# Kernel tuning notes

Hardware: AMD Instinct MI355X
Metric: run time of the kernel (lower is better)

## Reference

```python
import jax, jax.numpy as jnp
from jax import lax
import numpy as np

B, H, W, C = 4, 128, 128, 128   # C == d_route == n_heads, patch_len == H
OFFSET_RANGE = 5.0              # offset_range_factor == kernel == 5
SCALE = C ** -0.5               # self.scale_factor = d_route**-0.5
CYCLE = 168


def grid_sample_bilinear(img, grid):
    """torch.nn.functional.grid_sample(mode='bilinear', padding_mode='zeros', align_corners=False).
    img: (B,C,H,W); grid: (B,H,W,2) with (x,y) in [-1,1]."""
    Bn, Cn, Hn, Wn = img.shape
    xg = (grid[..., 0] + 1.0) * (Wn / 2.0) - 0.5
    yg = (grid[..., 1] + 1.0) * (Hn / 2.0) - 0.5
    x0 = jnp.floor(xg)
    y0 = jnp.floor(yg)
    img_flat = img.reshape(Bn, Cn, Hn * Wn)
    out = jnp.zeros_like(img)
    for xi in (x0, x0 + 1.0):
        for yi in (y0, y0 + 1.0):
            wgt = (1.0 - jnp.abs(xg - xi)) * (1.0 - jnp.abs(yg - yi))
            valid = (xi >= 0) & (xi <= Wn - 1) & (yi >= 0) & (yi <= Hn - 1)
            ix = jnp.clip(xi, 0, Wn - 1).astype(jnp.int32)
            iy = jnp.clip(yi, 0, Hn - 1).astype(jnp.int32)
            idx = (iy * Wn + ix).reshape(Bn, 1, -1)                      # (B,1,H*W)
            vals = jnp.take_along_axis(img_flat, idx, axis=2).reshape(Bn, Cn, Hn, Wn)
            out = out + vals * (wgt * valid.astype(img.dtype))[:, None, :, :]
    return out


def setup_inputs():
    key = jax.random.key(0)
    ks = jax.random.split(key, 12)
    s = C ** -0.5
    inp = {
        "x": jax.random.normal(ks[0], (B, H, W, C), dtype=jnp.float32),
        "cycle_index": jax.random.randint(ks[1], (B, 128), 0, CYCLE),  # dead path in cycle_mode='None'
        "Wq": jax.random.normal(ks[2], (C, C), dtype=jnp.float32) * s,
        "bq": jnp.zeros((C,), dtype=jnp.float32),
        "Wk": jax.random.normal(ks[3], (C, C), dtype=jnp.float32) * s,
        "bk": jnp.zeros((C,), dtype=jnp.float32),
        "Wv": jax.random.normal(ks[4], (C, C), dtype=jnp.float32) * s,
        "bv": jnp.zeros((C,), dtype=jnp.float32),
        "Wo": jax.random.normal(ks[5], (C, C), dtype=jnp.float32) * s,
        "bo": jnp.zeros((C,), dtype=jnp.float32),
        "Wc1": jax.random.normal(ks[6], (C, C, 5, 5), dtype=jnp.float32) * (1.0 / np.sqrt(C * 25)),
        "bc1": jnp.zeros((C,), dtype=jnp.float32),
        "Wc2": jax.random.normal(ks[7], (2, C), dtype=jnp.float32) * s,   # 1x1 conv, no bias
        "rel_bias": jax.random.normal(ks[8], (1, C, H, 1), dtype=jnp.float32) * 0.02,
    }
    return inp


def reference(x, cycle_index, Wq, bq, Wk, bk, Wv, bv, Wo, bo, Wc1, bc1, Wc2, rel_bias):
    Bn, Hn, Wn, Cn = x.shape
    xc = jnp.transpose(x, (0, 3, 1, 2))                                  # (B,C,H,W)
    # proj_q (1x1 conv) on x (cycle_mode='None')
    q = jnp.einsum('oc,bchw->bohw', Wq, xc) + bq[None, :, None, None]
    # proj_offset: 5x5 conv (pad 2) -> 1x1 conv to 2 channels, tanh * offset_range_factor
    c1 = lax.conv_general_dilated(q, Wc1, (1, 1), ((2, 2), (2, 2)),
                                  dimension_numbers=('NCHW', 'OIHW', 'NCHW')) + bc1[None, :, None, None]
    offset = jnp.tanh(jnp.einsum('oc,bchw->bohw', Wc2, c1)) * OFFSET_RANGE  # (B,2,H,W)
    # create_grid_like + normalize_grid (faithful, incl. x-coord normalized by H and vice versa)
    gx, gy = jnp.meshgrid(jnp.arange(Wn, dtype=x.dtype), jnp.arange(Hn, dtype=x.dtype), indexing='xy')
    grid = jnp.stack([gx, gy], axis=0)                                   # (2,H,W)
    vgrid = grid[None] + offset                                          # (B,2,H,W)
    gh = 2.0 * vgrid[:, 0] / max(Hn - 1, 1) - 1.0
    gw = 2.0 * vgrid[:, 1] / max(Wn - 1, 1) - 1.0
    sgrid = jnp.stack([gh, gw], axis=-1)                                 # (B,H,W,2) = (x,y) for grid_sample
    x_sampled = grid_sample_bilinear(xc, sgrid)                          # (B,C,H,W); n_groups=1 -> rearrange is identity
    k = (jnp.einsum('oc,bchw->bohw', Wk, x_sampled) + bk[None, :, None, None]).reshape(Bn * Cn, Hn, Wn)
    v = (jnp.einsum('oc,bchw->bohw', Wv, x_sampled) + bv[None, :, None, None] + rel_bias).reshape(Bn * Cn, Hn, Wn)
    qr = q.reshape(Bn * Cn, Hn, Wn)
    scores = jnp.einsum('bid,bjd->bij', qr, k) * SCALE                   # (B*C,H,H)
    attn = jax.nn.softmax(scores, axis=-1)
    out = jnp.einsum('bij,bjd->bid', attn, v)                            # (B*C,H,W)
    out = out.reshape(Bn, Hn, Wn, Cn)                                    # faithful raw reshape (as in original)
    return out @ Wo.T + bo
```

## Files before the change

kernel.cpp:

```cpp
#include <hip/hip_runtime.h>
#include <math.h>

#define IMG 16384

typedef short short4v __attribute__((ext_vector_type(4)));
typedef short short8  __attribute__((ext_vector_type(8)));
typedef float floatx4 __attribute__((ext_vector_type(4)));

__device__ __forceinline__ float4 ld4(const float* p) {
    return *reinterpret_cast<const float4*>(p);
}
__device__ __forceinline__ short f2bf(float f) {
    union { float f; unsigned u; } v; v.f = f;
    unsigned r = v.u + 0x7fffu + ((v.u >> 16) & 1u);
    return (short)(r >> 16);
}
__device__ __forceinline__ float bf2f(short s) {
    union { unsigned u; float f; } v;
    v.u = ((unsigned)(unsigned short)s) << 16;
    return v.f;
}

__launch_bounds__(256)
__global__ void k_wprep(const float* __restrict__ Wc1, const float* __restrict__ Wc2,
                        const float* __restrict__ bc1, const float* __restrict__ Wq,
                        const float* __restrict__ bq, const float* __restrict__ Wk,
                        const float* __restrict__ Wv, const float* __restrict__ Wo,
                        float* __restrict__ W2, float* __restrict__ cst,
                        float* __restrict__ b_eff, short* __restrict__ wbf) {
    const int t = threadIdx.x;
    if (blockIdx.x >= 50) {
        int i = (blockIdx.x - 50) * 256 + t;
        int base = i * 8;
        int sel = base >> 14, off = base & 16383;
        const float* s = (sel == 0) ? Wq : (sel == 1) ? Wk : (sel == 2) ? Wv : Wo;
        float4 a = ld4(s + off), b = ld4(s + off + 4);
        short8 o;
        o[0] = f2bf(a.x); o[1] = f2bf(a.y); o[2] = f2bf(a.z); o[3] = f2bf(a.w);
        o[4] = f2bf(b.x); o[5] = f2bf(b.y); o[6] = f2bf(b.z); o[7] = f2bf(b.w);
        *reinterpret_cast<short8*>(wbf + base) = o;
        return;
    }
    __shared__ float U[128];
    __shared__ float red[256];
    __shared__ float wc2[128];
    __shared__ float bql[128];
    const int tt = blockIdx.x;
    const int tch = tt / 25, tap = tt % 25;
    if (t < 128) { wc2[t] = Wc2[tch * 128 + t]; bql[t] = bq[t]; }
    __syncthreads();
    const int c = t & 127, half = t >> 7;
    float p = 0.f;
    for (int o = half * 64; o < half * 64 + 64; ++o)
        p += wc2[o] * Wc1[(o * 128 + c) * 25 + tap];
    red[half * 128 + c] = p;
    __syncthreads();
    if (t < 128) U[t] = red[t] + red[128 + t];
    __syncthreads();
    float p2 = 0.f;
    for (int cc = half * 64; cc < half * 64 + 64; ++cc)
        p2 += U[cc] * Wq[cc * 128 + c];
    red[half * 128 + c] = p2;
    __syncthreads();
    if (t < 128) W2[tt * 128 + t] = red[t] + red[128 + t];
    if (t < 128) red[t] = U[t] * bql[t];
    __syncthreads();
    if (t == 0) {
        float s = 0.f;
        for (int j = 0; j < 128; ++j) s += red[j];
        cst[tt] = s;
    }
    if (tap == 0) {
        __syncthreads();
        if (t < 128) red[t] = wc2[t] * bc1[t];
        __syncthreads();
        if (t == 0) {
            float s = 0.f;
            for (int j = 0; j < 128; ++j) s += red[j];
            b_eff[tch] = s;
        }
    }
}

__launch_bounds__(256)
__global__ void k_off(const float* __restrict__ x, const float* __restrict__ W2,
                      const float* __restrict__ cst, float* __restrict__ P,
                      short* __restrict__ x_bf) {
    __shared__ float Wlds[128 * 68];
    __shared__ float Alds[32 * 68];
    const int t = threadIdx.x;
    const int pg = t & 15, og = t >> 4;
    const int p0 = blockIdx.x * 64;
    const int b = p0 >> 14, pix0 = p0 & (IMG - 1);

    for (int id = t; id < 128 * 64; id += 256) {
        int k = id >> 6, o = id & 63;
        Wlds[k * 68 + o] = (o < 50) ? W2[o * 128 + k] : 0.f;
    }
    float acc[4][4];
#pragma unroll
    for (int i = 0; i < 4; ++i)
#pragma unroll
        for (int j = 0; j < 4; ++j) acc[i][j] = 0.f;

    for (int kc = 0; kc < 128; kc += 32) {
        __syncthreads();
#pragma unroll
        for (int rep = 0; rep < 2; ++rep) {
            int id = rep * 256 + t;
            int m = id >> 3, k4 = (id & 7) * 4;
            float4 v = ld4(x + (size_t)(p0 + m) * 128 + kc + k4);
            Alds[(k4 + 0) * 68 + m] = v.x;
            Alds[(k4 + 1) * 68 + m] = v.y;
            Alds[(k4 + 2) * 68 + m] = v.z;
            Alds[(k4 + 3) * 68 + m] = v.w;
            short4v s = {f2bf(v.x), f2bf(v.y), f2bf(v.z), f2bf(v.w)};
            *reinterpret_cast<short4v*>(x_bf + (size_t)(p0 + m) * 128 + kc + k4) = s;
        }
        __syncthreads();
#pragma unroll
        for (int k = 0; k < 32; ++k) {
            float4 a = *reinterpret_cast<float4*>(&Alds[k * 68 + 4 * pg]);
            float4 wv = *reinterpret_cast<float4*>(&Wlds[(kc + k) * 68 + 4 * og]);
            float av[4] = {a.x, a.y, a.z, a.w};
            float wf[4] = {wv.x, wv.y, wv.z, wv.w};
#pragma unroll
            for (int i = 0; i < 4; ++i)
#pragma unroll
                for (int j = 0; j < 4; ++j)
                    acc[i][j] = fmaf(av[i], wf[j], acc[i][j]);
        }
    }
    __syncthreads();
#pragma unroll
    for (int j = 0; j < 4; ++j) {
        int o = 4 * og + j;
        float c = (o < 50) ? cst[o] : 0.f;
        *reinterpret_cast<float4*>(&Wlds[o * 68 + 4 * pg]) =
            make_float4(acc[0][j] + c, acc[1][j] + c, acc[2][j] + c, acc[3][j] + c);
    }
    __syncthreads();
    for (int id = t; id < 50 * 16; id += 256) {
        int o = id >> 4, px4 = (id & 15) * 4;
        float4 v = *reinterpret_cast<float4*>(&Wlds[o * 68 + px4]);
        *reinterpret_cast<float4*>(P + ((size_t)(b * 50 + o)) * IMG + pix0 + px4) = v;
    }
}

__launch_bounds__(256, 2)
__global__ void k_fused2(const float* __restrict__ P, const float* __restrict__ b_eff,
                         const short* __restrict__ x_bf, const short* __restrict__ wbf,
                         const float* __restrict__ bq, const float* __restrict__ bk,
                         const float* __restrict__ bv, const float* __restrict__ rel,
                         short* __restrict__ q_bf, short* __restrict__ k_bf,
                         short* __restrict__ v_bf) {
    __shared__ __align__(16) char smem[62240];
    float* rowsP  = (float*)smem;
    short* xsT    = (short*)(smem + 26400);
    float* offs_l = (float*)(smem + 61216);

    const int t = threadIdx.x;
    const int w = t >> 6, l = t & 63, l15 = l & 15, quad = l >> 4;
    const int mh = w >> 1, nh = w & 1;
    const int bh = blockIdx.x;
    const int b = bh >> 7, h = bh & 127;

    for (int id = t; id < 1600; id += 256) {
        int o = id >> 5, q4 = (id & 31) * 4;
        int di = (o % 25) / 5;
        int r = h + di - 2;
        float4 v = make_float4(0.f, 0.f, 0.f, 0.f);
        if (r >= 0 && r < 128)
            v = ld4(P + ((size_t)(b * 50 + o)) * IMG + r * 128 + q4);
        *reinterpret_cast<float4*>(&rowsP[o * 132 + q4]) = v;
    }
    __syncthreads();
    {
        int wp = t & 127, tc = t >> 7;
        float acc = 0.f;
#pragma unroll
        for (int di = 0; di < 5; ++di)
#pragma unroll
            for (int dj = 0; dj < 5; ++dj) {
                int wj = wp + dj - 2;
                if (wj >= 0 && wj < 128)
                    acc += rowsP[(tc * 25 + di * 5 + dj) * 132 + wj];
            }
        offs_l[tc * 128 + wp] = tanhf(acc + b_eff[tc]) * 5.0f;
    }
    __syncthreads();

    for (int id = t; id < 2048; id += 256) {
        int px = id >> 4, c8 = id & 15;
        float ox = offs_l[px];
        float oy = offs_l[128 + px];
        float xg = ((float)px + ox) * (128.0f / 127.0f) - 0.5f;
        float yg = ((float)h  + oy) * (128.0f / 127.0f) - 0.5f;
        float x0f = floorf(xg), y0f = floorf(yg);
        float fx = xg - x0f, fy = yg - y0f;
        int x0 = (int)x0f, y0 = (int)y0f;
        float s[8];
#pragma unroll
        for (int r = 0; r < 8; ++r) s[r] = 0.f;
#pragma unroll
        for (int tap = 0; tap < 4; ++tap) {
            int xi = x0 + (tap & 1), yi = y0 + (tap >> 1);
            float wgt = ((tap & 1) ? fx : 1.f - fx) * ((tap >> 1) ? fy : 1.f - fy);
            if (xi >= 0 && xi < 128 && yi >= 0 && yi < 128) {
                short8 v = *reinterpret_cast<const short8*>(
                    x_bf + (((size_t)(b * 128 + yi)) * 128 + xi) * 128 + c8 * 8);
#pragma unroll
                for (int r = 0; r < 8; ++r) s[r] = fmaf(wgt, bf2f(v[r]), s[r]);
            }
        }
        short8 o;
#pragma unroll
        for (int r = 0; r < 8; ++r) o[r] = f2bf(s[r]);
        *reinterpret_cast<short8*>(&xsT[px * 136 + c8 * 8]) = o;
    }

    {
        const short* xr = x_bf + ((size_t)(b * 128 + h)) * 128 * 128;
        floatx4 acc[4][4];
#pragma unroll
        for (int im = 0; im < 4; ++im)
#pragma unroll
            for (int in = 0; in < 4; ++in)
                acc[im][in] = (floatx4){0.f, 0.f, 0.f, 0.f};
#pragma unroll
        for (int kc = 0; kc < 128; kc += 32) {
            short8 af[4], bf_[4];
#pragma unroll
            for (int im = 0; im < 4; ++im)
                af[im] = *reinterpret_cast<const short8*>(
                    xr + (mh * 64 + im * 16 + l15) * 128 + kc + quad * 8);
#pragma unroll
            for (int in = 0; in < 4; ++in)
                bf_[in] = *reinterpret_cast<const short8*>(
                    wbf + (nh * 64 + in * 16 + l15) * 128 + kc + quad * 8);
#pragma unroll
            for (int im = 0; im < 4; ++im)
#pragma unroll
                for (int in = 0; in < 4; ++in)
                    acc[im][in] = __builtin_amdgcn_mfma_f32_16x16x32_bf16(
                        af[im], bf_[in], acc[im][in], 0, 0, 0);
        }
#pragma unroll
        for (int in = 0; in < 4; ++in) {
            int o = nh * 64 + in * 16 + l15;
            float bb = bq[o];
#pragma unroll
            for (int im = 0; im < 4; ++im) {
                int px0 = mh * 64 + im * 16 + quad * 4;
                short4v s = {f2bf(acc[im][in][0] + bb), f2bf(acc[im][in][1] + bb),
                             f2bf(acc[im][in][2] + bb), f2bf(acc[im][in][3] + bb)};
                *reinterpret_cast<short4v*>(
                    q_bf + ((size_t)(b * 128 + o)) * IMG + h * 128 + px0) = s;
            }
        }
    }
    __syncthreads();

    {
        floatx4 ak[4][4], av[4][4];
#pragma unroll
        for (int im = 0; im < 4; ++im)
#pragma unroll
            for (int in = 0; in < 4; ++in) {
                ak[im][in] = (floatx4){0.f, 0.f, 0.f, 0.f};
                av[im][in] = (floatx4){0.f, 0.f, 0.f, 0.f};
            }
#pragma unroll
        for (int kc = 0; kc < 128; kc += 32) {
            short8 af[4], bk_[4], bv_[4];
#pragma unroll
            for (int im = 0; im < 4; ++im)
                af[im] = *reinterpret_cast<const short8*>(
                    &xsT[(mh * 64 + im * 16 + l15) * 136 + kc + quad * 8]);
#pragma unroll
            for (int in = 0; in < 4; ++in) {
                bk_[in] = *reinterpret_cast<const short8*>(
                    wbf + 16384 + (nh * 64 + in * 16 + l15) * 128 + kc + quad * 8);
                bv_[in] = *reinterpret_cast<const short8*>(
                    wbf + 32768 + (nh * 64 + in * 16 + l15) * 128 + kc + quad * 8);
            }
#pragma unroll
            for (int im = 0; im < 4; ++im)
#pragma unroll
                for (int in = 0; in < 4; ++in) {
                    ak[im][in] = __builtin_amdgcn_mfma_f32_16x16x32_bf16(
                        af[im], bk_[in], ak[im][in], 0, 0, 0);
                    av[im][in] = __builtin_amdgcn_mfma_f32_16x16x32_bf16(
                        af[im], bv_[in], av[im][in], 0, 0, 0);
                }
        }
#pragma unroll
        for (int in = 0; in < 4; ++in) {
            int o = nh * 64 + in * 16 + l15;
            float bbk = bk[o];
            float bbv = bv[o] + rel[o * 128 + h];
#pragma unroll
            for (int im = 0; im < 4; ++im) {
                int px0 = mh * 64 + im * 16 + quad * 4;
                size_t base = ((size_t)(b * 128 + o)) * IMG + h * 128 + px0;
                short4v sk = {f2bf(ak[im][in][0] + bbk), f2bf(ak[im][in][1] + bbk),
                              f2bf(ak[im][in][2] + bbk), f2bf(ak[im][in][3] + bbk)};
                short4v sv = {f2bf(av[im][in][0] + bbv), f2bf(av[im][in][1] + bbv),
                              f2bf(av[im][in][2] + bbv), f2bf(av[im][in][3] + bbv)};
                *reinterpret_cast<short4v*>(k_bf + base) = sk;
                *reinterpret_cast<short4v*>(v_bf + base) = sv;
            }
        }
    }
}

__launch_bounds__(256)
__global__ void k_attn3(const short* __restrict__ q_bf, const short* __restrict__ k_bf,
                        const short* __restrict__ v_bf, const short* __restrict__ WoB,
                        const float* __restrict__ bo, float* __restrict__ outp) {
    __shared__ __align__(16) short Pb[128 * 136];
    __shared__ __align__(16) short vT[128 * 136];
    __shared__ float redm[2 * 128];
    __shared__ float reds[2 * 128];

    const int t = threadIdx.x;
    const int w = t >> 6, l = t & 63, l15 = l & 15, quad = l >> 4;
    const int mh = w >> 1, nh = w & 1;
    const size_t hb = (size_t)blockIdx.x * IMG;
    const short* qp = q_bf + hb;
    const short* kp = k_bf + hb;
    const short* vp = v_bf + hb;

    for (int id = t; id < 2048; id += 256) {
        int j = id >> 4, seg = id & 15;
        short8 v8 = *reinterpret_cast<const short8*>(vp + j * 128 + seg * 8);
#pragma unroll
        for (int r = 0; r < 8; ++r)
            vT[(seg * 8 + r) * 136 + j] = v8[r];
    }

    floatx4 acc[4][4];
#pragma unroll
    for (int im = 0; im < 4; ++im)
#pragma unroll
        for (int in = 0; in < 4; ++in)
            acc[im][in] = (floatx4){0.f, 0.f, 0.f, 0.f};

#pragma unroll
    for (int kc = 0; kc < 128; kc += 32) {
        short8 af[4], bf_[4];
#pragma unroll
        for (int im = 0; im < 4; ++im)
            af[im] = *reinterpret_cast<const short8*>(
                qp + (mh * 64 + im * 16 + l15) * 128 + kc + quad * 8);
#pragma unroll
        for (int in = 0; in < 4; ++in)
            bf_[in] = *reinterpret_cast<const short8*>(
                kp + (nh * 64 + in * 16 + l15) * 128 + kc + quad * 8);
#pragma unroll
        for (int im = 0; im < 4; ++im)
#pragma unroll
            for (int in = 0; in < 4; ++in)
                acc[im][in] = __builtin_amdgcn_mfma_f32_16x16x32_bf16(
                    af[im], bf_[in], acc[im][in], 0, 0, 0);
    }

    const float scale = 0.08838834764831845f;
    float mloc[4][4];
#pragma unroll
    for (int im = 0; im < 4; ++im)
#pragma unroll
        for (int r = 0; r < 4; ++r) {
            float m = acc[im][0][r];
#pragma unroll
            for (int in = 1; in < 4; ++in) m = fmaxf(m, acc[im][in][r]);
            mloc[im][r] = m;
        }
#pragma unroll
    for (int mask = 1; mask < 16; mask <<= 1)
#pragma unroll
        for (int im = 0; im < 4; ++im)
#pragma unroll
            for (int r = 0; r < 4; ++r)
                mloc[im][r] = fmaxf(mloc[im][r], __shfl_xor(mloc[im][r], mask, 64));
    if (l15 == 0) {
#pragma unroll
        for (int im = 0; im < 4; ++im)
#pragma unroll
            for (int r = 0; r < 4; ++r)
                redm[nh * 128 + mh * 64 + im * 16 + quad * 4 + r] = mloc[im][r];
    }
    __syncthreads();
    float sloc[4][4];
#pragma unroll
    for (int im = 0; im < 4; ++im)
#pragma unroll
        for (int r = 0; r < 4; ++r) {
            int row = mh * 64 + im * 16 + quad * 4 + r;
            float m = fmaxf(redm[row], redm[128 + row]);
            float ss = 0.f;
#pragma unroll
            for (int in = 0; in < 4; ++in) {
                float e = __expf((acc[im][in][r] - m) * scale);
                acc[im][in][r] = e;
                ss += e;
            }
            sloc[im][r] = ss;
        }
#pragma unroll
    for (int mask = 1; mask < 16; mask <<= 1)
#pragma unroll
        for (int im = 0; im < 4; ++im)
#pragma unroll
            for (int r = 0; r < 4; ++r)
                sloc[im][r] += __shfl_xor(sloc[im][r], mask, 64);
    if (l15 == 0) {
#pragma unroll
        for (int im = 0; im < 4; ++im)
#pragma unroll
            for (int r = 0; r < 4; ++r)
                reds[nh * 128 + mh * 64 + im * 16 + quad * 4 + r] = sloc[im][r];
    }
    __syncthreads();
#pragma unroll
    for (int im = 0; im < 4; ++im)
#pragma unroll
        for (int r = 0; r < 4; ++r) {
            int row = mh * 64 + im * 16 + quad * 4 + r;
            float inv = 1.0f / (reds[row] + reds[128 + row]);
#pragma unroll
            for (int in = 0; in < 4; ++in) {
                int col = nh * 64 + in * 16 + l15;
                Pb[row * 136 + col] = f2bf(acc[im][in][r] * inv);
            }
        }
    __syncthreads();

#pragma unroll
    for (int im = 0; im < 4; ++im)
#pragma unroll
        for (int in = 0; in < 4; ++in)
            acc[im][in] = (floatx4){0.f, 0.f, 0.f, 0.f};
#pragma unroll
    for (int kc = 0; kc < 128; kc += 32) {
        short8 af[4], bf_[4];
#pragma unroll
        for (int im = 0; im < 4; ++im)
            af[im] = *reinterpret_cast<const short8*>(
                &Pb[(mh * 64 + im * 16 + l15) * 136 + kc + quad * 8]);
#pragma unroll
        for (int in = 0; in < 4; ++in)
            bf_[in] = *reinterpret_cast<const short8*>(
                &vT[(nh * 64 + in * 16 + l15) * 136 + kc + quad * 8]);
#pragma unroll
        for (int im = 0; im < 4; ++im)
#pragma unroll
            for (int in = 0; in < 4; ++in)
                acc[im][in] = __builtin_amdgcn_mfma_f32_16x16x32_bf16(
                    af[im], bf_[in], acc[im][in], 0, 0, 0);
    }
    __syncthreads();
#pragma unroll
    for (int im = 0; im < 4; ++im)
#pragma unroll
        for (int in = 0; in < 4; ++in) {
            int col = nh * 64 + in * 16 + l15;
#pragma unroll
            for (int r = 0; r < 4; ++r) {
                int row = mh * 64 + im * 16 + quad * 4 + r;
                Pb[row * 136 + col] = f2bf(acc[im][in][r]);
            }
        }
    __syncthreads();

    float bb[4];
#pragma unroll
    for (int in = 0; in < 4; ++in) bb[in] = bo[nh * 64 + in * 16 + l15];
#pragma unroll
    for (int im = 0; im < 4; ++im)
#pragma unroll
        for (int in = 0; in < 4; ++in)
            acc[im][in] = (floatx4){0.f, 0.f, 0.f, 0.f};
#pragma unroll
    for (int kc = 0; kc < 128; kc += 32) {
        short8 af[4], bf_[4];
#pragma unroll
        for (int im = 0; im < 4; ++im)
            af[im] = *reinterpret_cast<const short8*>(
                &Pb[(mh * 64 + im * 16 + l15) * 136 + kc + quad * 8]);
#pragma unroll
        for (int in = 0; in < 4; ++in)
            bf_[in] = *reinterpret_cast<const short8*>(
                WoB + (nh * 64 + in * 16 + l15) * 128 + kc + quad * 8);
#pragma unroll
        for (int im = 0; im < 4; ++im)
#pragma unroll
            for (int in = 0; in < 4; ++in)
                acc[im][in] = __builtin_amdgcn_mfma_f32_16x16x32_bf16(
                    af[im], bf_[in], acc[im][in], 0, 0, 0);
    }
#pragma unroll
    for (int im = 0; im < 4; ++im)
#pragma unroll
        for (int in = 0; in < 4; ++in) {
            int col = nh * 64 + in * 16 + l15;
#pragma unroll
            for (int r = 0; r < 4; ++r) {
                int row = mh * 64 + im * 16 + quad * 4 + r;
                outp[hb + (size_t)row * 128 + col] = acc[im][in][r] + bb[in];
            }
        }
}

extern "C" void kernel_launch(void* const* d_in, const int* in_sizes, int n_in,
                              void* d_out, int out_size, void* d_ws, size_t ws_size,
                              hipStream_t stream) {
    const float* x   = (const float*)d_in[0];
    const float* Wq  = (const float*)d_in[2];
    const float* bq  = (const float*)d_in[3];
    const float* Wk  = (const float*)d_in[4];
    const float* bk  = (const float*)d_in[5];
    const float* Wv  = (const float*)d_in[6];
    const float* bv  = (const float*)d_in[7];
    const float* Wo  = (const float*)d_in[8];
    const float* bo  = (const float*)d_in[9];
    const float* Wc1 = (const float*)d_in[10];
    const float* bc1 = (const float*)d_in[11];
    const float* Wc2 = (const float*)d_in[12];
    const float* rel = (const float*)d_in[13];

    char* wsb = (char*)d_ws;
    short* q_bf  = (short*)(wsb);
    short* k_bf  = (short*)(wsb + 1ull * 16777216);
    short* v_bf  = (short*)(wsb + 2ull * 16777216);
    short* x_bf  = (short*)(wsb + 3ull * 16777216);
    float* P     = (float*)(wsb + 4ull * 16777216);
    float* W2    = (float*)(wsb + 4ull * 16777216 + 13107200);
    float* cst   = W2 + 6400;
    float* b_eff = cst + 64;
    short* wbf   = (short*)(b_eff + 16);
    float* outp  = (float*)d_out;

    hipLaunchKernelGGL(k_wprep,  dim3(82),   dim3(256), 0, stream, Wc1, Wc2, bc1, Wq, bq,
                       Wk, Wv, Wo, W2, cst, b_eff, wbf);
    hipLaunchKernelGGL(k_off,    dim3(1024), dim3(256), 0, stream, x, W2, cst, P, x_bf);
    hipLaunchKernelGGL(k_fused2, dim3(512),  dim3(256), 0, stream, P, b_eff, x_bf, wbf,
                       bq, bk, bv, rel, q_bf, k_bf, v_bf);
    hipLaunchKernelGGL(k_attn3,  dim3(512),  dim3(256), 0, stream, q_bf, k_bf, v_bf,
                       wbf + 49152, bo, outp);
}
```

Baseline: 236.5 us.

## Stage q/k/v projection outputs through LDS for coalesced stores; swizzle vT

```diff
diff --git a/kernel.cpp b/kernel.cpp
--- a/kernel.cpp
+++ b/kernel.cpp
@@ -148,16 +148,17 @@
 }
 
 __launch_bounds__(256, 2)
-__global__ void k_fused2(const float* __restrict__ P, const float* __restrict__ b_eff,
+__global__ void k_fused3(const float* __restrict__ P, const float* __restrict__ b_eff,
                          const short* __restrict__ x_bf, const short* __restrict__ wbf,
                          const float* __restrict__ bq, const float* __restrict__ bk,
                          const float* __restrict__ bv, const float* __restrict__ rel,
                          short* __restrict__ q_bf, short* __restrict__ k_bf,
                          short* __restrict__ v_bf) {
-    __shared__ __align__(16) char smem[62240];
+    __shared__ __align__(16) char smem[70656];
     float* rowsP  = (float*)smem;
-    short* xsT    = (short*)(smem + 26400);
-    float* offs_l = (float*)(smem + 61216);
+    short* stg    = (short*)smem;
+    short* xsT    = (short*)(smem + 34816);
+    float* offs_l = (float*)(smem + 69632);
 
     const int t = threadIdx.x;
     const int w = t >> 6, l = t & 63, l15 = l & 15, quad = l >> 4;
@@ -245,21 +246,27 @@
                     acc[im][in] = __builtin_amdgcn_mfma_f32_16x16x32_bf16(
                         af[im], bf_[in], acc[im][in], 0, 0, 0);
         }
+        __syncthreads();
 #pragma unroll
         for (int in = 0; in < 4; ++in) {
             int o = nh * 64 + in * 16 + l15;
             float bb = bq[o];
 #pragma unroll
             for (int im = 0; im < 4; ++im) {
-                int px0 = mh * 64 + im * 16 + quad * 4;
+                int row0 = mh * 64 + im * 16 + quad * 4;
                 short4v s = {f2bf(acc[im][in][0] + bb), f2bf(acc[im][in][1] + bb),
                              f2bf(acc[im][in][2] + bb), f2bf(acc[im][in][3] + bb)};
-                *reinterpret_cast<short4v*>(
-                    q_bf + ((size_t)(b * 128 + o)) * IMG + h * 128 + px0) = s;
-            }
-        }
-    }
-    __syncthreads();
+                *reinterpret_cast<short4v*>(&stg[o * 136 + row0]) = s;
+            }
+        }
+    }
+    __syncthreads();
+    for (int id = t; id < 2048; id += 256) {
+        int o = id >> 4, seg = id & 15;
+        *reinterpret_cast<short8*>(
+            q_bf + ((size_t)(b * 128 + o)) * IMG + h * 128 + seg * 8)
+            = *reinterpret_cast<const short8*>(&stg[o * 136 + seg * 8]);
+    }
 
     {
         floatx4 ak[4][4], av[4][4];
@@ -294,6 +301,7 @@
                         af[im], bv_[in], av[im][in], 0, 0, 0);
                 }
         }
+        __syncthreads();
 #pragma unroll
         for (int in = 0; in < 4; ++in) {
             int o = nh * 64 + in * 16 + l15;
@@ -301,20 +309,29 @@
             float bbv = bv[o] + rel[o * 128 + h];
 #pragma unroll
             for (int im = 0; im < 4; ++im) {
-                int px0 = mh * 64 + im * 16 + quad * 4;
-                size_t base = ((size_t)(b * 128 + o)) * IMG + h * 128 + px0;
+                int row0 = mh * 64 + im * 16 + quad * 4;
                 short4v sk = {f2bf(ak[im][in][0] + bbk), f2bf(ak[im][in][1] + bbk),
                               f2bf(ak[im][in][2] + bbk), f2bf(ak[im][in][3] + bbk)};
                 short4v sv = {f2bf(av[im][in][0] + bbv), f2bf(av[im][in][1] + bbv),
                               f2bf(av[im][in][2] + bbv), f2bf(av[im][in][3] + bbv)};
-                *reinterpret_cast<short4v*>(k_bf + base) = sk;
-                *reinterpret_cast<short4v*>(v_bf + base) = sv;
-            }
-        }
-    }
-}
-
-__launch_bounds__(256)
+                *reinterpret_cast<short4v*>(&stg[o * 136 + row0]) = sk;
+                *reinterpret_cast<short4v*>(&xsT[o * 136 + row0]) = sv;
+            }
+        }
+    }
+    __syncthreads();
+    for (int id = t; id < 4096; id += 256) {
+        int sel = id >> 11;
+        int o = (id >> 4) & 127, seg = id & 15;
+        short* dst = sel ? v_bf : k_bf;
+        const short* src = sel ? xsT : stg;
+        *reinterpret_cast<short8*>(
+            dst + ((size_t)(b * 128 + o)) * IMG + h * 128 + seg * 8)
+            = *reinterpret_cast<const short8*>(&src[o * 136 + seg * 8]);
+    }
+}
+
+__launch_bounds__(256, 2)
 __global__ void k_attn3(const short* __restrict__ q_bf, const short* __restrict__ k_bf,
                         const short* __restrict__ v_bf, const short* __restrict__ WoB,
                         const float* __restrict__ bo, float* __restrict__ outp) {
@@ -334,9 +351,11 @@
     for (int id = t; id < 2048; id += 256) {
         int j = id >> 4, seg = id & 15;
         short8 v8 = *reinterpret_cast<const short8*>(vp + j * 128 + seg * 8);
+        int cbase = ((j >> 3) ^ seg) & 15;
+        int off = j & 7;
 #pragma unroll
         for (int r = 0; r < 8; ++r)
-            vT[(seg * 8 + r) * 136 + j] = v8[r];
+            vT[(seg * 8 + r) * 136 + cbase * 8 + off] = v8[r];
     }
 
     floatx4 acc[4][4];
@@ -449,9 +468,12 @@
             af[im] = *reinterpret_cast<const short8*>(
                 &Pb[(mh * 64 + im * 16 + l15) * 136 + kc + quad * 8]);
 #pragma unroll
-        for (int in = 0; in < 4; ++in)
+        for (int in = 0; in < 4; ++in) {
+            int dRow = nh * 64 + in * 16 + l15;
+            int cphys = (((kc >> 3) + quad) ^ (dRow >> 3)) & 15;
             bf_[in] = *reinterpret_cast<const short8*>(
-                &vT[(nh * 64 + in * 16 + l15) * 136 + kc + quad * 8]);
+                &vT[dRow * 136 + cphys * 8]);
+        }
 #pragma unroll
         for (int im = 0; im < 4; ++im)
 #pragma unroll
@@ -544,7 +566,7 @@
     hipLaunchKernelGGL(k_wprep,  dim3(82),   dim3(256), 0, stream, Wc1, Wc2, bc1, Wq, bq,
                        Wk, Wv, Wo, W2, cst, b_eff, wbf);
     hipLaunchKernelGGL(k_off,    dim3(1024), dim3(256), 0, stream, x, W2, cst, P, x_bf);
-    hipLaunchKernelGGL(k_fused2, dim3(512),  dim3(256), 0, stream, P, b_eff, x_bf, wbf,
+    hipLaunchKernelGGL(k_fused3, dim3(512),  dim3(256), 0, stream, P, b_eff, x_bf, wbf,
                        bq, bk, bv, rel, q_bf, k_bf, v_bf);
     hipLaunchKernelGGL(k_attn3,  dim3(512),  dim3(256), 0, stream, q_bf, k_bf, v_bf,
                        wbf + 49152, bo, outp);
```

New measurement: 220.3 us. 6.8% less time.
